# Kernel optimization log

Measured on AMD Instinct MI355X. Metric: run time of the kernel, lower is better.

The kernel has to match this reference:

```python
import jax, jax.numpy as jnp
import numpy as np

N_HEAD = 8

def setup_inputs() -> dict:
    key = jax.random.key(0)
    ks = jax.random.split(key, 5)
    N, C, T, V = 64, 128, 64, 25
    x = jax.random.normal(ks[0], (N, C, T, V), dtype=jnp.float32)
    Wa = jax.random.normal(ks[1], (C, C), dtype=jnp.float32) * (1.0 / np.sqrt(C))
    ba = jax.random.normal(ks[2], (C,), dtype=jnp.float32) * 0.01
    Wp = jax.random.normal(ks[3], (C, C), dtype=jnp.float32) * (1.0 / np.sqrt(C))
    bp = jax.random.normal(ks[4], (C,), dtype=jnp.float32) * 0.01
    temp = jnp.ones((N_HEAD, 1), dtype=jnp.float32)
    denom_bias = jnp.zeros((N_HEAD, 1, 1), dtype=jnp.float32)
    return {"x": x, "Wa": Wa, "ba": ba, "Wp": Wp, "bp": bp, "temp": temp, "denom_bias": denom_bias}

def reference(x, Wa, ba, Wp, bp, temp, denom_bias):
    # x: (N, C, T, V); eval mode (dropout = identity); residual = identity (in==out, stride==1)
    N, C, T, V = x.shape
    H = N_HEAD
    hd = C // H
    res = x
    # 1x1 conv c_attn
    w = jnp.einsum('nctv,oc->notv', x, Wa) + ba[None, :, None, None]
    # (N,H,hd,T,V) -> (N,H,T,V,hd) -> (N,H,T*V,hd)
    w = w.reshape(N, H, hd, T, V).transpose(0, 1, 3, 4, 2).reshape(N, H, T * V, hd)
    w_sq = w * w
    denom = jnp.maximum(jnp.cumsum(w_sq, axis=2), 1e-12)
    w_normed = w_sq / denom + denom_bias  # denom_bias (H,1,1) broadcasts
    tmp = jnp.sum(w_normed, axis=-1) * temp  # (N,H,L) * (H,1)
    Pi = jax.nn.softmax(tmp, axis=2)  # (N,H,L)
    dots = jnp.cumsum(w_sq * Pi[..., None], axis=2) / (jnp.cumsum(Pi, axis=2) + 1e-8)[..., None]
    attn = 1.0 / (1.0 + dots)
    y = -(w * Pi[..., None]) * attn  # (N,H,L,hd)
    y = y.reshape(N, H, T, V, hd).transpose(0, 1, 4, 2, 3).reshape(N, C, T, V)
    y = jnp.einsum('nctv,oc->notv', y, Wp) + bp[None, :, None, None]
    y = y + res
    return jax.nn.relu(y)
```

## Files before the change

### kernel.cpp

```cpp
#include <hip/hip_runtime.h>
#include <hip/hip_bf16.h>

#define N_S     64
#define C_CH    128
#define L_SEQ   1600
#define H_HEADS 8
#define HD      16
#define SEGN    32
#define SEGL    50
#define PADW    136
#define PADT    72

typedef __attribute__((ext_vector_type(8))) short bf16x8;
typedef __attribute__((ext_vector_type(4))) float f32x4;

__device__ inline unsigned short f2bf(float f) {
  return __builtin_bit_cast(unsigned short, __float2bfloat16(f));
}
__device__ inline float bflo(unsigned int u) { return __builtin_bit_cast(float, u << 16); }
__device__ inline float bfhi(unsigned int u) { return __builtin_bit_cast(float, u & 0xffff0000u); }
__device__ inline unsigned int pk(float a, float b) {
  return (unsigned int)f2bf(a) | ((unsigned int)f2bf(b) << 16);
}

template <int CTRL>
__device__ inline float dppadd(float x) {
  int r = __builtin_amdgcn_update_dpp(0, __builtin_bit_cast(int, x), CTRL, 0xF, 0xF, true);
  return x + __builtin_bit_cast(float, r);
}

__global__ __launch_bounds__(256) void k_gemm1(const float* __restrict__ x,
                                               const float* __restrict__ Wa,
                                               const float* __restrict__ ba,
                                               unsigned short* __restrict__ w2) {
  __shared__ unsigned short was[128 * PADW];
  __shared__ unsigned short xs[128 * PADT];
  const int n = blockIdx.y;
  const int l0 = blockIdx.x * 64;
  const int t = threadIdx.x;
  const float* xn = x + (size_t)n * (C_CH * L_SEQ);

#pragma unroll
  for (int it = 0; it < 16; ++it) {
    int pos = it * 256 + t;
    int o = pos >> 5;
    int c4 = (pos & 31) << 2;
    float4 v = *reinterpret_cast<const float4*>(Wa + o * C_CH + c4);
    ushort4 u;
    u.x = f2bf(v.x); u.y = f2bf(v.y); u.z = f2bf(v.z); u.w = f2bf(v.w);
    *reinterpret_cast<ushort4*>(&was[o * PADW + c4]) = u;
  }
#pragma unroll
  for (int it = 0; it < 8; ++it) {
    int pos = it * 256 + t;
    int c = pos >> 4;
    int l4 = (pos & 15) << 2;
    float4 v = *reinterpret_cast<const float4*>(xn + (size_t)c * L_SEQ + l0 + l4);
    ushort4 u;
    u.x = f2bf(v.x); u.y = f2bf(v.y); u.z = f2bf(v.z); u.w = f2bf(v.w);
    *reinterpret_cast<ushort4*>(&xs[c * PADT + l4]) = u;
  }
  __syncthreads();

  const int wv = t >> 6;
  const int lane = t & 63;
  const int r16 = lane & 15;
  const int kg = lane >> 4;
  f32x4 acc[8];
#pragma unroll
  for (int ot = 0; ot < 8; ++ot) acc[ot] = (f32x4){0.f, 0.f, 0.f, 0.f};

#pragma unroll
  for (int ks = 0; ks < 4; ++ks) {
    bf16x8 a;
#pragma unroll
    for (int j = 0; j < 8; ++j)
      a[j] = (short)xs[(ks * 32 + kg * 8 + j) * PADT + wv * 16 + r16];
#pragma unroll
    for (int ot = 0; ot < 8; ++ot) {
      bf16x8 b = *reinterpret_cast<const bf16x8*>(&was[(ot * 16 + r16) * PADW + ks * 32 + kg * 8]);
      acc[ot] = __builtin_amdgcn_mfma_f32_16x16x32_bf16(a, b, acc[ot], 0, 0, 0);
    }
  }
#pragma unroll
  for (int ot = 0; ot < 8; ++ot) {
    float bav = ba[ot * 16 + r16];
    ushort4 u;
    u.x = f2bf(acc[ot][0] + bav);
    u.y = f2bf(acc[ot][1] + bav);
    u.z = f2bf(acc[ot][2] + bav);
    u.w = f2bf(acc[ot][3] + bav);
    size_t idx = (((size_t)n * H_HEADS + ot) * HD + r16) * L_SEQ + l0 + wv * 16 + kg * 4;
    *reinterpret_cast<ushort4*>(&w2[idx]) = u;
  }
}

__global__ __launch_bounds__(512, 4) void k_scan(const unsigned short* __restrict__ w2,
                                                 unsigned short* __restrict__ y2,
                                                 const float* __restrict__ temp,
                                                 const float* __restrict__ dbias) {
  __shared__ float stot[SEGN][17];
  __shared__ float red[8];

  const int nh = blockIdx.x;
  const int h = nh & 7;
  const int t = threadIdx.x;
  const int d = t & 15;
  const int lane = t & 63;
  const int wv = t >> 6;
  const int seg = t >> 4;
  const size_t base = ((size_t)nh * HD + d) * L_SEQ + seg * SEGL;
  const float tscale = temp[h];
  const float db16 = 16.f * dbias[h];
  const float M = fmaxf((16.f + db16) * tscale, db16 * tscale);

  unsigned int vp[25];
  {
    const unsigned int* src = reinterpret_cast<const unsigned int*>(w2 + base);
#pragma unroll
    for (int ii = 0; ii < 25; ++ii) vp[ii] = src[ii];
  }

  float tot = 0.f;
#pragma unroll
  for (int ii = 0; ii < 25; ++ii) {
    float a = bflo(vp[ii]), b = bfhi(vp[ii]);
    tot += a * a + b * b;
  }
  stot[seg][d] = tot;
  __syncthreads();
#pragma unroll
  for (int it = 0; it < 2; ++it) {
    int col = wv + it * 8;
    float val = (lane < 32) ? stot[lane][col] : 0.f;
#pragma unroll
    for (int sh = 1; sh < 32; sh <<= 1) {
      float nv = __shfl_up(val, sh);
      if (lane >= sh) val += nv;
    }
    if (lane < 32) stot[lane][col] = val;
  }
  __syncthreads();
  const float off = stot[seg][d] - tot;

  unsigned int ep[25];
  float run = off;
  float sAcc = 0.f, wpAcc = 0.f;
  float eprev = 0.f;
#pragma unroll
  for (int i = 0; i < SEGL; ++i) {
    float v = (i & 1) ? bfhi(vp[i >> 1]) : bflo(vp[i >> 1]);
    float wsq = v * v;
    run += wsq;
    float c = __fdividef(wsq, fmaxf(run, 1e-12f));
    c = dppadd<0x128>(c);
    c = dppadd<0x124>(c);
    c = dppadd<0x122>(c);
    c = dppadd<0x121>(c);
    float e = __expf((c + db16) * tscale - M);
    sAcc += e;
    wpAcc = fmaf(wsq, e, wpAcc);
    if (i & 1) ep[i >> 1] = pk(eprev, e); else eprev = e;
  }
  {
    float s = sAcc;
#pragma unroll
    for (int mask = 32; mask; mask >>= 1) s += __shfl_xor(s, mask);
    if (lane == 0) red[wv] = s;
  }
  __syncthreads();
  float S16 = 0.f;
#pragma unroll
  for (int i2 = 0; i2 < 8; ++i2) S16 += red[i2];
  const float S = S16 * 0.0625f;
  const float ninvS = -1.0f / S;
  const float epsS = 1e-8f * S;

  stot[seg][d] = wpAcc;
  if (d == 0) stot[seg][16] = sAcc;
  __syncthreads();
#pragma unroll
  for (int it = 0; it < 2; ++it) {
    int col = wv + it * 8;
    float val = (lane < 32) ? stot[lane][col] : 0.f;
#pragma unroll
    for (int sh = 1; sh < 32; sh <<= 1) {
      float nv = __shfl_up(val, sh);
      if (lane >= sh) val += nv;
    }
    if (lane < 32) stot[lane][col] = val;
  }
  if (wv == 0) {
    float val = (lane < 32) ? stot[lane][16] : 0.f;
#pragma unroll
    for (int sh = 1; sh < 32; sh <<= 1) {
      float nv = __shfl_up(val, sh);
      if (lane >= sh) val += nv;
    }
    if (lane < 32) stot[lane][16] = val;
  }
  __syncthreads();
  const float wp_off = stot[seg][d] - wpAcc;
  const float pi_off = stot[seg][16] - sAcc;

  {
    float run_wp = wp_off, run_pi = pi_off;
    float ylo = 0.f;
#pragma unroll
    for (int i = 0; i < SEGL; ++i) {
      float v = (i & 1) ? bfhi(vp[i >> 1]) : bflo(vp[i >> 1]);
      float e = (i & 1) ? bfhi(ep[i >> 1]) : bflo(ep[i >> 1]);
      run_pi += e;
      run_wp = fmaf(v * v, e, run_wp);
      float dn = run_pi + epsS;
      float y = (v * e) * __fdividef(dn, dn + run_wp) * ninvS;
      if (i & 1) vp[i >> 1] = pk(ylo, y); else ylo = y;
    }
  }
  {
    unsigned int* dst = reinterpret_cast<unsigned int*>(y2 + base);
#pragma unroll
    for (int ii = 0; ii < 25; ++ii) dst[ii] = vp[ii];
  }
}

__global__ __launch_bounds__(256) void k_gemm2(const unsigned short* __restrict__ y2,
                                               const float* __restrict__ Wp,
                                               const float* __restrict__ bp,
                                               const float* __restrict__ x,
                                               float* __restrict__ out) {
  __shared__ unsigned short wps[128 * PADW];
  __shared__ unsigned short ys[128 * PADT];
  const int n = blockIdx.y;
  const int l0 = blockIdx.x * 64;
  const int t = threadIdx.x;

#pragma unroll
  for (int it = 0; it < 16; ++it) {
    int pos = it * 256 + t;
    int o = pos >> 5;
    int c4 = (pos & 31) << 2;
    float4 v = *reinterpret_cast<const float4*>(Wp + o * C_CH + c4);
    ushort4 u;
    u.x = f2bf(v.x); u.y = f2bf(v.y); u.z = f2bf(v.z); u.w = f2bf(v.w);
    *reinterpret_cast<ushort4*>(&wps[o * PADW + c4]) = u;
  }
#pragma unroll
  for (int it = 0; it < 4; ++it) {
    int pos = it * 256 + t;
    int c = pos >> 3;
    int l8 = (pos & 7) << 3;
    uint4 v = *reinterpret_cast<const uint4*>(y2 + ((size_t)n * C_CH + c) * L_SEQ + l0 + l8);
    *reinterpret_cast<uint4*>(&ys[c * PADT + l8]) = v;
  }
  __syncthreads();

  const int wv = t >> 6;
  const int lane = t & 63;
  const int r16 = lane & 15;
  const int kg = lane >> 4;
  f32x4 acc[8];
#pragma unroll
  for (int ot = 0; ot < 8; ++ot) acc[ot] = (f32x4){0.f, 0.f, 0.f, 0.f};

#pragma unroll
  for (int ks = 0; ks < 4; ++ks) {
    bf16x8 b;
#pragma unroll
    for (int j = 0; j < 8; ++j)
      b[j] = (short)ys[(ks * 32 + kg * 8 + j) * PADT + wv * 16 + r16];
#pragma unroll
    for (int ot = 0; ot < 8; ++ot) {
      bf16x8 a = *reinterpret_cast<const bf16x8*>(&wps[(ot * 16 + r16) * PADW + ks * 32 + kg * 8]);
      acc[ot] = __builtin_amdgcn_mfma_f32_16x16x32_bf16(a, b, acc[ot], 0, 0, 0);
    }
  }
  const int gl = l0 + wv * 16 + r16;
#pragma unroll
  for (int ot = 0; ot < 8; ++ot) {
#pragma unroll
    for (int i = 0; i < 4; ++i) {
      int o = ot * 16 + kg * 4 + i;
      size_t idx = (size_t)n * (C_CH * L_SEQ) + (size_t)o * L_SEQ + gl;
      float r = acc[ot][i] + bp[o] + x[idx];
      out[idx] = fmaxf(r, 0.f);
    }
  }
}

extern "C" void kernel_launch(void* const* d_in, const int* in_sizes, int n_in,
                              void* d_out, int out_size, void* d_ws, size_t ws_size,
                              hipStream_t stream) {
  const float* x     = (const float*)d_in[0];
  const float* Wa    = (const float*)d_in[1];
  const float* ba    = (const float*)d_in[2];
  const float* Wp    = (const float*)d_in[3];
  const float* bp    = (const float*)d_in[4];
  const float* temp  = (const float*)d_in[5];
  const float* dbias = (const float*)d_in[6];
  float* out = (float*)d_out;

  unsigned short* w2 = (unsigned short*)d_ws;
  unsigned short* y2 = w2 + (size_t)N_S * H_HEADS * L_SEQ * HD;

  k_gemm1<<<dim3(L_SEQ / 64, N_S), 256, 0, stream>>>(x, Wa, ba, w2);
  k_scan<<<N_S * H_HEADS, 512, 0, stream>>>(w2, y2, temp, dbias);
  k_gemm2<<<dim3(L_SEQ / 64, N_S), 256, 0, stream>>>(y2, Wp, bp, x, out);
}
```

Baseline: 76.85 us.

## Interleave intermediate layout so scan loads and stores coalesce across threads

```diff
diff --git a/kernel.cpp b/kernel.cpp
--- a/kernel.cpp
+++ b/kernel.cpp
@@ -9,7 +9,8 @@
 #define SEGN    32
 #define SEGL    50
 #define PADW    136
-#define PADT    72
+#define PADT    70
+#define NHQ     12800
 
 typedef __attribute__((ext_vector_type(8))) short bf16x8;
 typedef __attribute__((ext_vector_type(4))) float f32x4;
@@ -29,10 +30,11 @@
   return x + __builtin_bit_cast(float, r);
 }
 
+
 __global__ __launch_bounds__(256) void k_gemm1(const float* __restrict__ x,
                                                const float* __restrict__ Wa,
                                                const float* __restrict__ ba,
-                                               unsigned short* __restrict__ w2) {
+                                               unsigned int* __restrict__ w3) {
   __shared__ unsigned short was[128 * PADW];
   __shared__ unsigned short xs[128 * PADT];
   const int n = blockIdx.y;
@@ -82,21 +84,26 @@
       acc[ot] = __builtin_amdgcn_mfma_f32_16x16x32_bf16(a, b, acc[ot], 0, 0, 0);
     }
   }
+  const int lbase = l0 + wv * 16 + kg * 4;
+  const unsigned int lp0 = (unsigned int)lbase >> 1;
+  const unsigned int seg0 = lp0 / 25u;
+  const unsigned int ii0 = lp0 - seg0 * 25u;
+  const unsigned int seg1 = (ii0 == 24u) ? seg0 + 1u : seg0;
+  const unsigned int ii1 = (ii0 == 24u) ? 0u : ii0 + 1u;
+  const unsigned int off0 = ii0 * 512u + seg0 * 16u + (unsigned int)r16;
+  const unsigned int off1 = ii1 * 512u + seg1 * 16u + (unsigned int)r16;
+  unsigned int* w3n = w3 + (size_t)(n * H_HEADS) * NHQ;
 #pragma unroll
   for (int ot = 0; ot < 8; ++ot) {
     float bav = ba[ot * 16 + r16];
-    ushort4 u;
-    u.x = f2bf(acc[ot][0] + bav);
-    u.y = f2bf(acc[ot][1] + bav);
-    u.z = f2bf(acc[ot][2] + bav);
-    u.w = f2bf(acc[ot][3] + bav);
-    size_t idx = (((size_t)n * H_HEADS + ot) * HD + r16) * L_SEQ + l0 + wv * 16 + kg * 4;
-    *reinterpret_cast<ushort4*>(&w2[idx]) = u;
-  }
-}
-
-__global__ __launch_bounds__(512, 4) void k_scan(const unsigned short* __restrict__ w2,
-                                                 unsigned short* __restrict__ y2,
+    unsigned int* p = w3n + (size_t)ot * NHQ;
+    p[off0] = pk(acc[ot][0] + bav, acc[ot][1] + bav);
+    p[off1] = pk(acc[ot][2] + bav, acc[ot][3] + bav);
+  }
+}
+
+__global__ __launch_bounds__(512, 8) void k_scan(const unsigned int* __restrict__ w3,
+                                                 unsigned int* __restrict__ y3,
                                                  const float* __restrict__ temp,
                                                  const float* __restrict__ dbias) {
   __shared__ float stot[SEGN][17];
@@ -109,17 +116,14 @@
   const int lane = t & 63;
   const int wv = t >> 6;
   const int seg = t >> 4;
-  const size_t base = ((size_t)nh * HD + d) * L_SEQ + seg * SEGL;
   const float tscale = temp[h];
   const float db16 = 16.f * dbias[h];
   const float M = fmaxf((16.f + db16) * tscale, db16 * tscale);
 
   unsigned int vp[25];
-  {
-    const unsigned int* src = reinterpret_cast<const unsigned int*>(w2 + base);
-#pragma unroll
-    for (int ii = 0; ii < 25; ++ii) vp[ii] = src[ii];
-  }
+  const unsigned int* srcd = w3 + (size_t)nh * NHQ;
+#pragma unroll
+  for (int ii = 0; ii < 25; ++ii) vp[ii] = srcd[ii * 512 + t];
 
   float tot = 0.f;
 #pragma unroll
@@ -217,14 +221,12 @@
       if (i & 1) vp[i >> 1] = pk(ylo, y); else ylo = y;
     }
   }
-  {
-    unsigned int* dst = reinterpret_cast<unsigned int*>(y2 + base);
-#pragma unroll
-    for (int ii = 0; ii < 25; ++ii) dst[ii] = vp[ii];
-  }
-}
-
-__global__ __launch_bounds__(256) void k_gemm2(const unsigned short* __restrict__ y2,
+  unsigned int* dstd = y3 + (size_t)nh * NHQ;
+#pragma unroll
+  for (int ii = 0; ii < 25; ++ii) dstd[ii * 512 + t] = vp[ii];
+}
+
+__global__ __launch_bounds__(256) void k_gemm2(const unsigned int* __restrict__ y3,
                                                const float* __restrict__ Wp,
                                                const float* __restrict__ bp,
                                                const float* __restrict__ x,
@@ -245,13 +247,17 @@
     u.x = f2bf(v.x); u.y = f2bf(v.y); u.z = f2bf(v.z); u.w = f2bf(v.w);
     *reinterpret_cast<ushort4*>(&wps[o * PADW + c4]) = u;
   }
-#pragma unroll
-  for (int it = 0; it < 4; ++it) {
-    int pos = it * 256 + t;
-    int c = pos >> 3;
-    int l8 = (pos & 7) << 3;
-    uint4 v = *reinterpret_cast<const uint4*>(y2 + ((size_t)n * C_CH + c) * L_SEQ + l0 + l8);
-    *reinterpret_cast<uint4*>(&ys[c * PADT + l8]) = v;
+  const int lpb = l0 >> 1;
+#pragma unroll
+  for (int k = 0; k < 16; ++k) {
+    int e = k * 256 + t;
+    int lpl = e >> 7;
+    int hd = e & 127;
+    unsigned int lp = (unsigned int)(lpb + lpl);
+    unsigned int sg = lp / 25u;
+    unsigned int ii = lp - sg * 25u;
+    unsigned int vdw = y3[(size_t)(n * H_HEADS + (hd >> 4)) * NHQ + ii * 512u + sg * 16u + (hd & 15)];
+    *reinterpret_cast<unsigned int*>(&ys[hd * PADT + 2 * lpl]) = vdw;
   }
   __syncthreads();
 
@@ -300,10 +306,10 @@
   const float* dbias = (const float*)d_in[6];
   float* out = (float*)d_out;
 
-  unsigned short* w2 = (unsigned short*)d_ws;
-  unsigned short* y2 = w2 + (size_t)N_S * H_HEADS * L_SEQ * HD;
-
-  k_gemm1<<<dim3(L_SEQ / 64, N_S), 256, 0, stream>>>(x, Wa, ba, w2);
-  k_scan<<<N_S * H_HEADS, 512, 0, stream>>>(w2, y2, temp, dbias);
-  k_gemm2<<<dim3(L_SEQ / 64, N_S), 256, 0, stream>>>(y2, Wp, bp, x, out);
-}
+  unsigned int* w3 = (unsigned int*)d_ws;
+  unsigned int* y3 = w3 + (size_t)N_S * H_HEADS * NHQ;
+
+  k_gemm1<<<dim3(L_SEQ / 64, N_S), 256, 0, stream>>>(x, Wa, ba, w3);
+  k_scan<<<N_S * H_HEADS, 512, 0, stream>>>(w3, y3, temp, dbias);
+  k_gemm2<<<dim3(L_SEQ / 64, N_S), 256, 0, stream>>>(y3, Wp, bp, x, out);
+}
```

After: 197.3 us. +156.7%, slower.

## Interleave scan workspace layout for coalesced loads and use 1024-thread scan blocks

Applied to the files above, without the earlier changes.

```diff
diff --git a/kernel.cpp b/kernel.cpp
--- a/kernel.cpp
+++ b/kernel.cpp
@@ -6,10 +6,12 @@
 #define L_SEQ   1600
 #define H_HEADS 8
 #define HD      16
-#define SEGN    32
-#define SEGL    50
+#define SEGN    64
+#define SEGL    25
 #define PADW    136
-#define PADT    72
+#define PADT    70
+#define NHD     13312
+#define NHU     26624
 
 typedef __attribute__((ext_vector_type(8))) short bf16x8;
 typedef __attribute__((ext_vector_type(4))) float f32x4;
@@ -29,10 +31,11 @@
   return x + __builtin_bit_cast(float, r);
 }
 
+
 __global__ __launch_bounds__(256) void k_gemm1(const float* __restrict__ x,
                                                const float* __restrict__ Wa,
                                                const float* __restrict__ ba,
-                                               unsigned short* __restrict__ w2) {
+                                               unsigned short* __restrict__ w3u) {
   __shared__ unsigned short was[128 * PADW];
   __shared__ unsigned short xs[128 * PADT];
   const int n = blockIdx.y;
@@ -82,25 +85,32 @@
       acc[ot] = __builtin_amdgcn_mfma_f32_16x16x32_bf16(a, b, acc[ot], 0, 0, 0);
     }
   }
+  const int lbase = l0 + wv * 16 + kg * 4;
+  unsigned int idxA[4];
+#pragma unroll
+  for (int i = 0; i < 4; ++i) {
+    unsigned int l = (unsigned int)(lbase + i);
+    unsigned int sg = l / 25u;
+    unsigned int j = l - sg * 25u;
+    idxA[i] = (j >> 1) * 2048u + sg * 32u + ((unsigned int)r16 << 1) + (j & 1u);
+  }
+  unsigned short* w3n = w3u + (size_t)(n * H_HEADS) * NHU;
 #pragma unroll
   for (int ot = 0; ot < 8; ++ot) {
     float bav = ba[ot * 16 + r16];
-    ushort4 u;
-    u.x = f2bf(acc[ot][0] + bav);
-    u.y = f2bf(acc[ot][1] + bav);
-    u.z = f2bf(acc[ot][2] + bav);
-    u.w = f2bf(acc[ot][3] + bav);
-    size_t idx = (((size_t)n * H_HEADS + ot) * HD + r16) * L_SEQ + l0 + wv * 16 + kg * 4;
-    *reinterpret_cast<ushort4*>(&w2[idx]) = u;
-  }
-}
-
-__global__ __launch_bounds__(512, 4) void k_scan(const unsigned short* __restrict__ w2,
-                                                 unsigned short* __restrict__ y2,
-                                                 const float* __restrict__ temp,
-                                                 const float* __restrict__ dbias) {
+    unsigned short* p = w3n + (size_t)ot * NHU;
+#pragma unroll
+    for (int i = 0; i < 4; ++i)
+      p[idxA[i]] = f2bf(acc[ot][i] + bav);
+  }
+}
+
+__global__ __launch_bounds__(1024) void k_scan(const unsigned int* __restrict__ w3d,
+                                               unsigned int* __restrict__ y3d,
+                                               const float* __restrict__ temp,
+                                               const float* __restrict__ dbias) {
   __shared__ float stot[SEGN][17];
-  __shared__ float red[8];
+  __shared__ float red[16];
 
   const int nh = blockIdx.x;
   const int h = nh & 7;
@@ -109,41 +119,38 @@
   const int lane = t & 63;
   const int wv = t >> 6;
   const int seg = t >> 4;
-  const size_t base = ((size_t)nh * HD + d) * L_SEQ + seg * SEGL;
   const float tscale = temp[h];
   const float db16 = 16.f * dbias[h];
   const float M = fmaxf((16.f + db16) * tscale, db16 * tscale);
-
-  unsigned int vp[25];
+  const float A = tscale * 1.44269504088896f;
+  const float B = (db16 * tscale - M) * 1.44269504088896f;
+
+  unsigned int vp[13];
+  const unsigned int* srcd = w3d + (size_t)nh * NHD;
+#pragma unroll
+  for (int ii = 0; ii < 13; ++ii) vp[ii] = srcd[ii * 1024 + t];
+
+  float tot = 0.f;
+#pragma unroll
+  for (int i = 0; i < SEGL; ++i) {
+    float v = (i & 1) ? bfhi(vp[i >> 1]) : bflo(vp[i >> 1]);
+    tot += v * v;
+  }
+  stot[seg][d] = tot;
+  __syncthreads();
   {
-    const unsigned int* src = reinterpret_cast<const unsigned int*>(w2 + base);
-#pragma unroll
-    for (int ii = 0; ii < 25; ++ii) vp[ii] = src[ii];
-  }
-
-  float tot = 0.f;
-#pragma unroll
-  for (int ii = 0; ii < 25; ++ii) {
-    float a = bflo(vp[ii]), b = bfhi(vp[ii]);
-    tot += a * a + b * b;
-  }
-  stot[seg][d] = tot;
-  __syncthreads();
-#pragma unroll
-  for (int it = 0; it < 2; ++it) {
-    int col = wv + it * 8;
-    float val = (lane < 32) ? stot[lane][col] : 0.f;
-#pragma unroll
-    for (int sh = 1; sh < 32; sh <<= 1) {
+    float val = stot[lane][wv];
+#pragma unroll
+    for (int sh = 1; sh < 64; sh <<= 1) {
       float nv = __shfl_up(val, sh);
       if (lane >= sh) val += nv;
     }
-    if (lane < 32) stot[lane][col] = val;
+    stot[lane][wv] = val;
   }
   __syncthreads();
   const float off = stot[seg][d] - tot;
 
-  unsigned int ep[25];
+  unsigned int ep[13];
   float run = off;
   float sAcc = 0.f, wpAcc = 0.f;
   float eprev = 0.f;
@@ -157,11 +164,12 @@
     c = dppadd<0x124>(c);
     c = dppadd<0x122>(c);
     c = dppadd<0x121>(c);
-    float e = __expf((c + db16) * tscale - M);
+    float e = exp2f(fmaf(c, A, B));
     sAcc += e;
     wpAcc = fmaf(wsq, e, wpAcc);
     if (i & 1) ep[i >> 1] = pk(eprev, e); else eprev = e;
   }
+  ep[12] = pk(eprev, 0.f);
   {
     float s = sAcc;
 #pragma unroll
@@ -171,7 +179,7 @@
   __syncthreads();
   float S16 = 0.f;
 #pragma unroll
-  for (int i2 = 0; i2 < 8; ++i2) S16 += red[i2];
+  for (int i2 = 0; i2 < 16; ++i2) S16 += red[i2];
   const float S = S16 * 0.0625f;
   const float ninvS = -1.0f / S;
   const float epsS = 1e-8f * S;
@@ -179,25 +187,23 @@
   stot[seg][d] = wpAcc;
   if (d == 0) stot[seg][16] = sAcc;
   __syncthreads();
-#pragma unroll
-  for (int it = 0; it < 2; ++it) {
-    int col = wv + it * 8;
-    float val = (lane < 32) ? stot[lane][col] : 0.f;
-#pragma unroll
-    for (int sh = 1; sh < 32; sh <<= 1) {
+  {
+    float val = stot[lane][wv];
+#pragma unroll
+    for (int sh = 1; sh < 64; sh <<= 1) {
       float nv = __shfl_up(val, sh);
       if (lane >= sh) val += nv;
     }
-    if (lane < 32) stot[lane][col] = val;
-  }
-  if (wv == 0) {
-    float val = (lane < 32) ? stot[lane][16] : 0.f;
-#pragma unroll
-    for (int sh = 1; sh < 32; sh <<= 1) {
-      float nv = __shfl_up(val, sh);
-      if (lane >= sh) val += nv;
-    }
-    if (lane < 32) stot[lane][16] = val;
+    stot[lane][wv] = val;
+    if (wv == 0) {
+      float val2 = stot[lane][16];
+#pragma unroll
+      for (int sh = 1; sh < 64; sh <<= 1) {
+        float nv = __shfl_up(val2, sh);
+        if (lane >= sh) val2 += nv;
+      }
+      stot[lane][16] = val2;
+    }
   }
   __syncthreads();
   const float wp_off = stot[seg][d] - wpAcc;
@@ -216,15 +222,14 @@
       float y = (v * e) * __fdividef(dn, dn + run_wp) * ninvS;
       if (i & 1) vp[i >> 1] = pk(ylo, y); else ylo = y;
     }
-  }
-  {
-    unsigned int* dst = reinterpret_cast<unsigned int*>(y2 + base);
-#pragma unroll
-    for (int ii = 0; ii < 25; ++ii) dst[ii] = vp[ii];
-  }
-}
-
-__global__ __launch_bounds__(256) void k_gemm2(const unsigned short* __restrict__ y2,
+    vp[12] = pk(ylo, 0.f);
+  }
+  unsigned int* dstd = y3d + (size_t)nh * NHD;
+#pragma unroll
+  for (int ii = 0; ii < 13; ++ii) dstd[ii * 1024 + t] = vp[ii];
+}
+
+__global__ __launch_bounds__(256) void k_gemm2(const unsigned short* __restrict__ y3u,
                                                const float* __restrict__ Wp,
                                                const float* __restrict__ bp,
                                                const float* __restrict__ x,
@@ -246,12 +251,16 @@
     *reinterpret_cast<ushort4*>(&wps[o * PADW + c4]) = u;
   }
 #pragma unroll
-  for (int it = 0; it < 4; ++it) {
-    int pos = it * 256 + t;
-    int c = pos >> 3;
-    int l8 = (pos & 7) << 3;
-    uint4 v = *reinterpret_cast<const uint4*>(y2 + ((size_t)n * C_CH + c) * L_SEQ + l0 + l8);
-    *reinterpret_cast<uint4*>(&ys[c * PADT + l8]) = v;
+  for (int k = 0; k < 32; ++k) {
+    int e = k * 256 + t;
+    int lloc = e >> 7;
+    int c = e & 127;
+    unsigned int l = (unsigned int)(l0 + lloc);
+    unsigned int sg = l / 25u;
+    unsigned int j = l - sg * 25u;
+    unsigned short v = y3u[(size_t)(n * H_HEADS + (c >> 4)) * NHU +
+                           (j >> 1) * 2048u + sg * 32u + ((unsigned int)(c & 15) << 1) + (j & 1u)];
+    ys[c * PADT + lloc] = v;
   }
   __syncthreads();
 
@@ -300,10 +309,10 @@
   const float* dbias = (const float*)d_in[6];
   float* out = (float*)d_out;
 
-  unsigned short* w2 = (unsigned short*)d_ws;
-  unsigned short* y2 = w2 + (size_t)N_S * H_HEADS * L_SEQ * HD;
-
-  k_gemm1<<<dim3(L_SEQ / 64, N_S), 256, 0, stream>>>(x, Wa, ba, w2);
-  k_scan<<<N_S * H_HEADS, 512, 0, stream>>>(w2, y2, temp, dbias);
-  k_gemm2<<<dim3(L_SEQ / 64, N_S), 256, 0, stream>>>(y2, Wp, bp, x, out);
-}
+  unsigned short* w3u = (unsigned short*)d_ws;
+  unsigned short* y3u = w3u + (size_t)N_S * H_HEADS * NHU;
+
+  k_gemm1<<<dim3(L_SEQ / 64, N_S), 256, 0, stream>>>(x, Wa, ba, w3u);
+  k_scan<<<N_S * H_HEADS, 1024, 0, stream>>>((const unsigned int*)w3u, (unsigned int*)y3u, temp, dbias);
+  k_gemm2<<<dim3(L_SEQ / 64, N_S), 256, 0, stream>>>(y3u, Wp, bp, x, out);
+}
```

Result: slower. 83.65 us (+8.9%).
